# Optimization experiments

Hardware: AMD Instinct MI355X
Metric: run time of the kernel (lower is better)

## Reference

```python
import jax, jax.numpy as jnp
import numpy as np

D = 128            # actual_dim / embed_dim
DM = 2 * D         # d_model
HID = 2 * DM       # LSTMCell hidden size
NSYM = 200000
PAD = NSYM
B = 4096
S = 5
NB = 64
STEPS = 4
EPS = 1e-6


def setup_inputs() -> dict:
    key = jax.random.key(0)
    ks = jax.random.split(key, 24)
    def rn(k, sh, scale=0.02):
        return jax.random.normal(k, sh, dtype=jnp.float32) * scale
    emb = rn(ks[10], (NSYM + 1, D)).at[PAD].set(0.0)  # padding row zeroed
    inp = {
        'query': jax.random.randint(ks[0], (B, 2), 0, NSYM),
        'support': jax.random.randint(ks[1], (S, 2), 0, NSYM),
        'q_l_conn': jax.random.randint(ks[2], (B, NB, 2), 0, NSYM),
        'q_l_deg': jax.random.randint(ks[3], (B,), 0, NB),
        'q_r_conn': jax.random.randint(ks[4], (B, NB, 2), 0, NSYM),
        'q_r_deg': jax.random.randint(ks[5], (B,), 0, NB),
        's_l_conn': jax.random.randint(ks[6], (S, NB, 2), 0, NSYM),
        's_l_deg': jax.random.randint(ks[7], (S,), 0, NB),
        's_r_conn': jax.random.randint(ks[8], (S, NB, 2), 0, NSYM),
        's_r_deg': jax.random.randint(ks[9], (S,), 0, NB),
        'emb': emb,
        'gcn_w': rn(ks[11], (D, 2 * D)),
        'gcn_bias': jnp.zeros((D,), jnp.float32),
        'proj1_w': rn(ks[12], (2 * DM, DM)),
        'proj1_b': jnp.zeros((2 * DM,), jnp.float32),
        'proj2_w': rn(ks[13], (DM, 2 * DM)),
        'proj2_b': jnp.zeros((DM,), jnp.float32),
        'ln_g': jnp.ones((DM,), jnp.float32),
        'ln_b': jnp.zeros((DM,), jnp.float32),
        'w_ih': rn(ks[14], (4 * HID, DM)),
        'w_hh': rn(ks[15], (4 * HID, HID)),
        'b_ih': jnp.zeros((4 * HID,), jnp.float32),
        'b_hh': jnp.zeros((4 * HID,), jnp.float32),
    }
    return inp


def _neighbor_encoder(conn, deg, emb, gcn_w, gcn_bias):
    # conn: [N, NB, 2] ids (rel, ent); deg: [N]
    rel = emb[conn[:, :, 0]]                     # [N, NB, D] gather
    ent = emb[conn[:, :, 1]]                     # [N, NB, D] gather
    x = jnp.concatenate([rel, ent], axis=-1)     # [N, NB, 2D]
    out = jnp.einsum('bnd,kd->bnk', x, gcn_w) + gcn_bias  # [N, NB, D]
    denom = jnp.maximum(deg, 1).astype(out.dtype)[:, None]
    return jnp.tanh(out.sum(axis=1) / denom)     # [N, D]


def _support_encoder(x, proj1_w, proj1_b, proj2_w, proj2_b, ln_g, ln_b):
    residual = x
    h = jax.nn.relu(x @ proj1_w.T + proj1_b)
    h = h @ proj2_w.T + proj2_b
    z = h + residual
    mu = z.mean(axis=-1, keepdims=True)
    sigma = jnp.std(z, axis=-1, keepdims=True, ddof=1)
    return ln_g * (z - mu) / (sigma + EPS) + ln_b


def _query_encoder(support_vec, query, w_ih, w_hh, b_ih, b_hh):
    # support_vec: [DM] (single support prototype); query: [B, DM]
    bsz = query.shape[0]
    h_r = jnp.zeros((bsz, HID), query.dtype)
    c = jnp.zeros((bsz, HID), query.dtype)
    xW = query @ w_ih.T + b_ih  # invariant across steps
    h = query
    for _ in range(STEPS):
        gates = xW + h_r @ w_hh.T + b_hh
        i, f, g, o = jnp.split(gates, 4, axis=-1)
        c = jax.nn.sigmoid(f) * c + jax.nn.sigmoid(i) * jnp.tanh(g)
        h_cell = jax.nn.sigmoid(o) * jnp.tanh(c)
        h = query + h_cell[:, :DM]
        # attention over a single support row: softmax of one logit == 1
        r = jnp.broadcast_to(support_vec[None, :], h.shape)
        h_r = jnp.concatenate([h, r], axis=-1)
    return h


def reference(query, support, q_l_conn, q_l_deg, q_r_conn, q_r_deg,
              s_l_conn, s_l_deg, s_r_conn, s_r_deg,
              emb, gcn_w, gcn_bias, proj1_w, proj1_b, proj2_w, proj2_b,
              ln_g, ln_b, w_ih, w_hh, b_ih, b_hh):
    ql = _neighbor_encoder(q_l_conn, q_l_deg, emb, gcn_w, gcn_bias)
    qr = _neighbor_encoder(q_r_conn, q_r_deg, emb, gcn_w, gcn_bias)
    sl = _neighbor_encoder(s_l_conn, s_l_deg, emb, gcn_w, gcn_bias)
    sr = _neighbor_encoder(s_r_conn, s_r_deg, emb, gcn_w, gcn_bias)
    query_nb = jnp.concatenate([ql, qr], axis=-1)    # [B, DM]
    support_nb = jnp.concatenate([sl, sr], axis=-1)  # [S, DM]
    se = lambda x: _support_encoder(x, proj1_w, proj1_b, proj2_w, proj2_b, ln_g, ln_b)
    support_g = se(support_nb).mean(axis=0)          # [DM]
    query_g = se(query_nb)                            # [B, DM]
    query_f = _query_encoder(support_g, query_g, w_ih, w_hh, b_ih, b_hh)
    qn = query_f / jnp.maximum(jnp.linalg.norm(query_f, axis=-1, keepdims=True), 1e-12)
    sn = support_g / jnp.maximum(jnp.linalg.norm(support_g), 1e-12)
    return qn @ sn                                    # [B] matching scores
```

## Files before the change

kernel.cpp:

```cpp
#include <hip/hip_runtime.h>

#define BQ 4096
#define NS 5

typedef __attribute__((ext_vector_type(8))) short bf16x8;
typedef __attribute__((ext_vector_type(4))) float f32x4;
typedef unsigned short ushortT;

#define WS_QNB    0
#define WS_Z      1048576
#define WS_QG     2097152
#define WS_XW     3145728
#define WS_CBUF   5242880
#define WS_XS     6291456
#define WS_H1B    7348224
#define WS_ABF    7872512
#define WS_HB1    8134656
#define WS_P1B    8396800
#define WS_P2B    8462336
#define WS_WIHB   8527872
#define WS_WHHB   8658944
#define WS_GWB    8790016
#define WS_SNB    8806400
#define WS_H1G    8807680
#define WS_ZB     8810240
#define WS_SG     8811520
#define WS_SN     8811776
#define WS_SWL    8812032
#define WS_BL     8813056

__device__ __forceinline__ float wave_allreduce(float v) {
#pragma unroll
  for (int off = 32; off > 0; off >>= 1) v += __shfl_xor(v, off, 64);
  return v;
}
__device__ __forceinline__ float block_allreduce(float v, float* buf) {
  v = wave_allreduce(v);
  __syncthreads();
  if ((threadIdx.x & 63) == 0) buf[threadIdx.x >> 6] = v;
  __syncthreads();
  return buf[0] + buf[1] + buf[2] + buf[3];
}
__device__ __forceinline__ float sigm(float x) { return 1.0f / (1.0f + expf(-x)); }
__device__ __forceinline__ ushortT f2bf(float f) {
  unsigned int u = __float_as_uint(f);
  unsigned int r = (u + 0x7fffu + ((u >> 16) & 1u)) >> 16;
  return (ushortT)r;
}
__device__ __forceinline__ float bf2f(ushortT u) {
  return __uint_as_float(((unsigned int)u) << 16);
}
__device__ __forceinline__ float dot4(float4 a, float4 b) {
  return a.x * b.x + a.y * b.y + a.z * b.z + a.w * b.w;
}

__global__ void k_pack(const float* __restrict__ w_ih, const float* __restrict__ w_hh,
                       const float* __restrict__ p1w, const float* __restrict__ p2w,
                       const float* __restrict__ gcn_w,
                       const float* __restrict__ b_ih, const float* __restrict__ b_hh,
                       ushortT* __restrict__ p1b16, ushortT* __restrict__ p2b16,
                       ushortT* __restrict__ wihb, ushortT* __restrict__ whhb,
                       ushortT* __restrict__ gwb, float* __restrict__ bL) {
  const int stride = gridDim.x * blockDim.x;
  const int gid = blockIdx.x * blockDim.x + threadIdx.x;
  for (int i = gid; i < 131072; i += stride) p1b16[i] = f2bf(p1w[i]);
  for (int i = gid; i < 131072; i += stride) p2b16[i] = f2bf(p2w[i]);
  for (int i = gid; i < 262144; i += stride) {
    int n = i >> 8, k = i & 255;
    int j = (n >> 2) + 512 * (n & 3);
    wihb[i] = f2bf(w_ih[j * 256 + k]);
    whhb[i] = f2bf(w_hh[j * 512 + k]);
  }
  for (int i = gid; i < 32768; i += stride) gwb[i] = f2bf(gcn_w[i]);
  for (int i = gid; i < 1024; i += stride) {
    int j = (i >> 2) + 512 * (i & 3);
    bL[i] = b_ih[j] + b_hh[j];
  }
}

__global__ __launch_bounds__(256) void k_gather(
    const int* __restrict__ qlc, const int* __restrict__ qrc,
    const int* __restrict__ slc, const int* __restrict__ src_,
    const float* __restrict__ emb, ushortT* __restrict__ XS) {
  const int r = blockIdx.x;
  const int b = r >> 1, side = r & 1;
  const int t = threadIdx.x;
  const int* cg;
  if (b < BQ) cg = (side ? qrc : qlc) + (size_t)b * 128;
  else        cg = (side ? src_ : slc) + (size_t)(b - BQ) * 128;
  __shared__ int connS[128];
  __shared__ __align__(16) float part[8][132];
  if (t < 128) connS[t] = cg[t];
  __syncthreads();
  const int s = t >> 5, l = t & 31;
  const float4* emb4 = (const float4*)emb;
  float4 acc = make_float4(0.f, 0.f, 0.f, 0.f);
#pragma unroll
  for (int kb = 0; kb < 2; kb++) {
    int im[8];
#pragma unroll
    for (int k = 0; k < 8; k++) im[k] = connS[(kb * 8 + k) * 8 + s];
    float4 v[8];
#pragma unroll
    for (int k = 0; k < 8; k++) v[k] = emb4[(size_t)im[k] * 32 + l];
#pragma unroll
    for (int k = 0; k < 8; k++) {
      acc.x += v[k].x; acc.y += v[k].y; acc.z += v[k].z; acc.w += v[k].w;
    }
  }
  *(float4*)&part[s][l * 4] = acc;
  __syncthreads();
  const int hf = t >> 7, dd = t & 127;
  float sum = part[hf][dd] + part[2 + hf][dd] + part[4 + hf][dd] + part[6 + hf][dd];
  XS[(size_t)r * 256 + t] = f2bf(sum);
}

__global__ __launch_bounds__(256) void k_gcn(
    const ushortT* __restrict__ XS, const ushortT* __restrict__ gwb,
    const float* __restrict__ gcn_bias,
    const int* __restrict__ qld, const int* __restrict__ qrd,
    const int* __restrict__ sld, const int* __restrict__ srd,
    float* __restrict__ qnb, float* __restrict__ snb, ushortT* __restrict__ xq) {
  __shared__ short As[64 * 40];
  __shared__ short Bs[128 * 40];
  __shared__ int degl[32], degr[32];
  const int t = threadIdx.x;
  const int row0 = blockIdx.x * 64;
  if (t < 32) {
    int b = (row0 >> 1) + t;
    int dl = 1, dr = 1;
    if (b < BQ) { dl = qld[b]; dr = qrd[b]; }
    else if (b < BQ + NS) { dl = sld[b - BQ]; dr = srd[b - BQ]; }
    degl[t] = (dl > 0) ? dl : 1;
    degr[t] = (dr > 0) ? dr : 1;
  }
  const int wave = t >> 6, lane = t & 63;
  const int wm = wave >> 1, wn = wave & 1, quad = lane >> 4, mr = lane & 15;
  f32x4 acc[2][4];
#pragma unroll
  for (int mi = 0; mi < 2; mi++)
#pragma unroll
    for (int ni = 0; ni < 4; ni++) acc[mi][ni] = (f32x4){0.f, 0.f, 0.f, 0.f};
  const int arow = t >> 2, akc = t & 3;
  for (int k0 = 0; k0 < 256; k0 += 32) {
    float4 av = *(const float4*)(XS + (size_t)(row0 + arow) * 256 + k0 + akc * 8);
    float4 bv0 = *(const float4*)(gwb + (size_t)arow * 256 + k0 + akc * 8);
    float4 bv1 = *(const float4*)(gwb + (size_t)(64 + arow) * 256 + k0 + akc * 8);
    __syncthreads();
    *(float4*)&As[arow * 40 + akc * 8] = av;
    *(float4*)&Bs[arow * 40 + akc * 8] = bv0;
    *(float4*)&Bs[(64 + arow) * 40 + akc * 8] = bv1;
    __syncthreads();
    bf16x8 af[2], bfr[4];
#pragma unroll
    for (int mi = 0; mi < 2; mi++)
      af[mi] = *(const bf16x8*)&As[(wm * 32 + mi * 16 + mr) * 40 + quad * 8];
#pragma unroll
    for (int ni = 0; ni < 4; ni++)
      bfr[ni] = *(const bf16x8*)&Bs[(wn * 64 + ni * 16 + mr) * 40 + quad * 8];
#pragma unroll
    for (int mi = 0; mi < 2; mi++)
#pragma unroll
      for (int ni = 0; ni < 4; ni++)
        acc[mi][ni] = __builtin_amdgcn_mfma_f32_16x16x32_bf16(af[mi], bfr[ni], acc[mi][ni], 0, 0, 0);
  }
#pragma unroll
  for (int mi = 0; mi < 2; mi++) {
#pragma unroll
    for (int ni = 0; ni < 4; ni++) {
      const int col = wn * 64 + ni * 16 + mr;
      const int rb = row0 + wm * 32 + mi * 16 + quad * 4;
      const float bs = 64.0f * gcn_bias[col];
#pragma unroll
      for (int reg = 0; reg < 4; reg++) {
        const int row = rb + reg;
        const int b = row >> 1, side = row & 1;
        if (b >= BQ + NS) continue;
        const int li = (row >> 1) - (row0 >> 1);
        const int deg = side ? degr[li] : degl[li];
        float val = tanhf((acc[mi][ni][reg] + bs) / (float)deg);
        if (b < BQ) {
          const size_t o = (size_t)b * 256 + side * 128 + col;
          qnb[o] = val;
          xq[o] = f2bf(val);
        } else {
          snb[(size_t)(b - BQ) * 256 + side * 128 + col] = val;
        }
      }
    }
  }
}

__global__ __launch_bounds__(256) void k_sup1(
    const float* __restrict__ snb, const float* __restrict__ p1w,
    const float* __restrict__ p1b, float* __restrict__ h1g) {
  const int w = blockIdx.x * 4 + (threadIdx.x >> 6);
  const int lane = threadIdx.x & 63;
  const int r = w >> 9, j = w & 511;
  float4 x = *(const float4*)&snb[r * 256 + lane * 4];
  float4 wv = *(const float4*)&p1w[(size_t)j * 256 + lane * 4];
  float s = wave_allreduce(dot4(x, wv));
  if (lane == 0) h1g[r * 512 + j] = fmaxf(s + p1b[j], 0.f);
}

__global__ __launch_bounds__(256) void k_sup2(
    const float* __restrict__ snb, const float* __restrict__ h1g,
    const float* __restrict__ p2w, const float* __restrict__ p2b,
    float* __restrict__ zb) {
  const int w = blockIdx.x * 4 + (threadIdx.x >> 6);
  const int lane = threadIdx.x & 63;
  const int r = w >> 8, tt = w & 255;
  float4 h0 = *(const float4*)&h1g[r * 512 + lane * 4];
  float4 h1 = *(const float4*)&h1g[r * 512 + 256 + lane * 4];
  float4 w0 = *(const float4*)&p2w[(size_t)tt * 512 + lane * 4];
  float4 w1 = *(const float4*)&p2w[(size_t)tt * 512 + 256 + lane * 4];
  float s = wave_allreduce(dot4(h0, w0) + dot4(h1, w1));
  if (lane == 0) zb[r * 256 + tt] = s + p2b[tt] + snb[r * 256 + tt];
}

__global__ __launch_bounds__(256) void k_sup3(
    const float* __restrict__ zb, const float* __restrict__ ln_g,
    const float* __restrict__ ln_b, float* __restrict__ sg, float* __restrict__ sn) {
  const int t = threadIdx.x;
  __shared__ float rbuf[4];
  float acc = 0.f;
  for (int r = 0; r < NS; r++) {
    float z = zb[r * 256 + t];
    float s = block_allreduce(z, rbuf);
    float mu = s * (1.f / 256.f);
    float dz = z - mu;
    float s2 = block_allreduce(dz * dz, rbuf);
    float rstd = 1.f / (sqrtf(s2 * (1.f / 255.f)) + 1e-6f);
    acc += ln_g[t] * dz * rstd + ln_b[t];
    __syncthreads();
  }
  float g = acc * (1.f / (float)NS);
  sg[t] = g;
  float n2 = block_allreduce(g * g, rbuf);
  sn[t] = g / fmaxf(sqrtf(n2), 1e-12f);
}

__global__ __launch_bounds__(256) void k_sup4(
    const float* __restrict__ sg, const float* __restrict__ w_hh,
    float* __restrict__ sWl) {
  const int n = blockIdx.x * 4 + (threadIdx.x >> 6);
  const int lane = threadIdx.x & 63;
  const int j = (n >> 2) + 512 * (n & 3);
  float4 x = *(const float4*)&sg[lane * 4];
  float4 wv = *(const float4*)&w_hh[(size_t)j * 512 + 256 + lane * 4];
  float s = wave_allreduce(dot4(x, wv));
  if (lane == 0) sWl[n] = s;
}

__global__ __launch_bounds__(256) void k_gemm(
    const ushortT* __restrict__ A, const ushortT* __restrict__ B,
    const float* __restrict__ bias, const float* __restrict__ aux,
    float* __restrict__ outf, ushortT* __restrict__ outb,
    int K, int N, int nbn, int mode) {
  __shared__ short As[64 * 40];
  __shared__ short Bs[128 * 40];
  const int t = threadIdx.x;
  const int bn = blockIdx.x % nbn, bm = blockIdx.x / nbn;
  const int row0 = bm * 64, col0 = bn * 128;
  const int wave = t >> 6, lane = t & 63;
  const int wm = wave >> 1, wn = wave & 1, quad = lane >> 4, mr = lane & 15;
  f32x4 acc[2][4];
#pragma unroll
  for (int mi = 0; mi < 2; mi++)
#pragma unroll
    for (int ni = 0; ni < 4; ni++) acc[mi][ni] = (f32x4){0.f, 0.f, 0.f, 0.f};
  const int arow = t >> 2, akc = t & 3;
  for (int k0 = 0; k0 < K; k0 += 32) {
    float4 av = *(const float4*)(A + (size_t)(row0 + arow) * K + k0 + akc * 8);
    float4 bv0 = *(const float4*)(B + (size_t)(col0 + arow) * K + k0 + akc * 8);
    float4 bv1 = *(const float4*)(B + (size_t)(col0 + 64 + arow) * K + k0 + akc * 8);
    __syncthreads();
    *(float4*)&As[arow * 40 + akc * 8] = av;
    *(float4*)&Bs[arow * 40 + akc * 8] = bv0;
    *(float4*)&Bs[(64 + arow) * 40 + akc * 8] = bv1;
    __syncthreads();
    bf16x8 af[2], bfr[4];
#pragma unroll
    for (int mi = 0; mi < 2; mi++)
      af[mi] = *(const bf16x8*)&As[(wm * 32 + mi * 16 + mr) * 40 + quad * 8];
#pragma unroll
    for (int ni = 0; ni < 4; ni++)
      bfr[ni] = *(const bf16x8*)&Bs[(wn * 64 + ni * 16 + mr) * 40 + quad * 8];
#pragma unroll
    for (int mi = 0; mi < 2; mi++)
#pragma unroll
      for (int ni = 0; ni < 4; ni++)
        acc[mi][ni] = __builtin_amdgcn_mfma_f32_16x16x32_bf16(af[mi], bfr[ni], acc[mi][ni], 0, 0, 0);
  }
#pragma unroll
  for (int mi = 0; mi < 2; mi++) {
#pragma unroll
    for (int ni = 0; ni < 4; ni++) {
      const int col = col0 + wn * 64 + ni * 16 + mr;
      const int rb = row0 + wm * 32 + mi * 16 + quad * 4;
      const float bs = bias[col];
#pragma unroll
      for (int reg = 0; reg < 4; reg++) {
        const int row = rb + reg;
        const size_t off = (size_t)row * N + col;
        float v = acc[mi][ni][reg];
        if (mode == 0) outb[off] = f2bf(fmaxf(v + bs, 0.f));
        else outf[off] = v + bs + aux[off];
      }
    }
  }
}

__global__ __launch_bounds__(256) void k_gemm_lstm(
    const ushortT* __restrict__ A, const ushortT* __restrict__ B,
    const float* __restrict__ bL, const float* __restrict__ sWl,
    const float* __restrict__ qg, ushortT* __restrict__ xwb,
    float* __restrict__ cbuf, ushortT* __restrict__ hb_out, int phase) {
  __shared__ short As[64 * 40];
  __shared__ short Bs[128 * 40];
  __shared__ __align__(16) float Cs[64 * 132];
  const int t = threadIdx.x;
  const int bn = blockIdx.x & 7, bm = blockIdx.x >> 3;
  const int row0 = bm * 64, col0 = bn * 128;
  const int wave = t >> 6, lane = t & 63;
  const int wm = wave >> 1, wn = wave & 1, quad = lane >> 4, mr = lane & 15;
  f32x4 acc[2][4];
#pragma unroll
  for (int mi = 0; mi < 2; mi++)
#pragma unroll
    for (int ni = 0; ni < 4; ni++) acc[mi][ni] = (f32x4){0.f, 0.f, 0.f, 0.f};
  const int arow = t >> 2, akc = t & 3;
  for (int k0 = 0; k0 < 256; k0 += 32) {
    float4 av = *(const float4*)(A + (size_t)(row0 + arow) * 256 + k0 + akc * 8);
    float4 bv0 = *(const float4*)(B + (size_t)(col0 + arow) * 256 + k0 + akc * 8);
    float4 bv1 = *(const float4*)(B + (size_t)(col0 + 64 + arow) * 256 + k0 + akc * 8);
    __syncthreads();
    *(float4*)&As[arow * 40 + akc * 8] = av;
    *(float4*)&Bs[arow * 40 + akc * 8] = bv0;
    *(float4*)&Bs[(64 + arow) * 40 + akc * 8] = bv1;
    __syncthreads();
    bf16x8 af[2], bfr[4];
#pragma unroll
    for (int mi = 0; mi < 2; mi++)
      af[mi] = *(const bf16x8*)&As[(wm * 32 + mi * 16 + mr) * 40 + quad * 8];
#pragma unroll
    for (int ni = 0; ni < 4; ni++)
      bfr[ni] = *(const bf16x8*)&Bs[(wn * 64 + ni * 16 + mr) * 40 + quad * 8];
#pragma unroll
    for (int mi = 0; mi < 2; mi++)
#pragma unroll
      for (int ni = 0; ni < 4; ni++)
        acc[mi][ni] = __builtin_amdgcn_mfma_f32_16x16x32_bf16(af[mi], bfr[ni], acc[mi][ni], 0, 0, 0);
  }
#pragma unroll
  for (int mi = 0; mi < 2; mi++)
#pragma unroll
    for (int ni = 0; ni < 4; ni++)
#pragma unroll
      for (int reg = 0; reg < 4; reg++)
        Cs[(wm * 32 + mi * 16 + quad * 4 + reg) * 132 + wn * 64 + ni * 16 + mr] =
            acc[mi][ni][reg];
  __syncthreads();
  const int u = t & 31, grp = t >> 5;
  const int ugl = bn * 32 + u;
#pragma unroll
  for (int i = 0; i < 8; i++) {
    const int rl = grp * 8 + i;
    const int row = row0 + rl;
    const size_t o = (size_t)row * 256 + ugl;
    float4 gv = *(const float4*)&Cs[rl * 132 + u * 4];
    if (phase == 0) {
      float4 bb = *(const float4*)&bL[col0 + u * 4];
      gv.x += bb.x; gv.y += bb.y; gv.z += bb.z; gv.w += bb.w;
      float c0 = sigm(gv.x) * tanhf(gv.z);
      float h = qg[o] + sigm(gv.w) * tanhf(c0);
      cbuf[o] = c0;
      hb_out[o] = f2bf(h);
      float4 sv = *(const float4*)&sWl[col0 + u * 4];
      ushort4 xo;
      xo.x = f2bf(gv.x + sv.x); xo.y = f2bf(gv.y + sv.y);
      xo.z = f2bf(gv.z + sv.z); xo.w = f2bf(gv.w + sv.w);
      *(ushort4*)&xwb[(size_t)row * 1024 + col0 + u * 4] = xo;
    } else {
      ushort4 xv = *(const ushort4*)&xwb[(size_t)row * 1024 + col0 + u * 4];
      gv.x += bf2f(xv.x); gv.y += bf2f(xv.y);
      gv.z += bf2f(xv.z); gv.w += bf2f(xv.w);
      float c = sigm(gv.y) * cbuf[o] + sigm(gv.x) * tanhf(gv.z);
      float h = qg[o] + sigm(gv.w) * tanhf(c);
      if (phase == 2) {
        cbuf[o] = h;
      } else {
        cbuf[o] = c;
        hb_out[o] = f2bf(h);
      }
    }
  }
}

__global__ __launch_bounds__(256) void k_ln(
    const float* __restrict__ Z, const float* __restrict__ ln_g,
    const float* __restrict__ ln_b, float* __restrict__ qg, ushortT* __restrict__ qgb) {
  const int t = threadIdx.x;
  const int row = blockIdx.x * 4 + (t >> 6);
  const int lane = t & 63;
  float4 z = *(const float4*)&Z[(size_t)row * 256 + lane * 4];
  float s = wave_allreduce(z.x + z.y + z.z + z.w);
  float mu = s * (1.f / 256.f);
  float dx = z.x - mu, dy = z.y - mu, dz = z.z - mu, dw = z.w - mu;
  float s2 = wave_allreduce(dx * dx + dy * dy + dz * dz + dw * dw);
  float rstd = 1.f / (sqrtf(s2 * (1.f / 255.f)) + 1e-6f);
  float4 g = *(const float4*)&ln_g[lane * 4];
  float4 bb = *(const float4*)&ln_b[lane * 4];
  float4 o;
  o.x = g.x * dx * rstd + bb.x;
  o.y = g.y * dy * rstd + bb.y;
  o.z = g.z * dz * rstd + bb.z;
  o.w = g.w * dw * rstd + bb.w;
  *(float4*)&qg[(size_t)row * 256 + lane * 4] = o;
  ushort4 u;
  u.x = f2bf(o.x); u.y = f2bf(o.y); u.z = f2bf(o.z); u.w = f2bf(o.w);
  *(ushort4*)&qgb[(size_t)row * 256 + lane * 4] = u;
}

__global__ __launch_bounds__(256) void k_out(
    const float* __restrict__ hf, const float* __restrict__ sn, float* __restrict__ out) {
  const int t = threadIdx.x;
  const int row = blockIdx.x * 4 + (t >> 6);
  const int lane = t & 63;
  float4 h = *(const float4*)&hf[(size_t)row * 256 + lane * 4];
  float4 s = *(const float4*)&sn[lane * 4];
  float dt = wave_allreduce(dot4(h, s));
  float nr = wave_allreduce(dot4(h, h));
  if (lane == 0) out[row] = dt / fmaxf(sqrtf(nr), 1e-12f);
}

extern "C" void kernel_launch(void* const* d_in, const int* in_sizes, int n_in,
                              void* d_out, int out_size, void* d_ws, size_t ws_size,
                              hipStream_t stream) {
  const int* q_l_conn = (const int*)d_in[2];
  const int* q_l_deg  = (const int*)d_in[3];
  const int* q_r_conn = (const int*)d_in[4];
  const int* q_r_deg  = (const int*)d_in[5];
  const int* s_l_conn = (const int*)d_in[6];
  const int* s_l_deg  = (const int*)d_in[7];
  const int* s_r_conn = (const int*)d_in[8];
  const int* s_r_deg  = (const int*)d_in[9];
  const float* emb      = (const float*)d_in[10];
  const float* gcn_w    = (const float*)d_in[11];
  const float* gcn_bias = (const float*)d_in[12];
  const float* proj1_w  = (const float*)d_in[13];
  const float* proj1_b  = (const float*)d_in[14];
  const float* proj2_w  = (const float*)d_in[15];
  const float* proj2_b  = (const float*)d_in[16];
  const float* ln_g     = (const float*)d_in[17];
  const float* ln_b     = (const float*)d_in[18];
  const float* w_ih     = (const float*)d_in[19];
  const float* w_hh     = (const float*)d_in[20];
  const float* b_ih     = (const float*)d_in[21];
  const float* b_hh     = (const float*)d_in[22];

  float* ws = (float*)d_ws;
  float* qnb   = ws + WS_QNB;
  float* Z     = ws + WS_Z;
  float* qg    = ws + WS_QG;
  ushortT* xwb = (ushortT*)(ws + WS_XW);
  float* cbuf  = ws + WS_CBUF;
  ushortT* XS    = (ushortT*)(ws + WS_XS);
  ushortT* h1b   = (ushortT*)(ws + WS_H1B);
  ushortT* abf   = (ushortT*)(ws + WS_ABF);
  ushortT* hb1   = (ushortT*)(ws + WS_HB1);
  ushortT* p1b16 = (ushortT*)(ws + WS_P1B);
  ushortT* p2b16 = (ushortT*)(ws + WS_P2B);
  ushortT* wihb  = (ushortT*)(ws + WS_WIHB);
  ushortT* whhb  = (ushortT*)(ws + WS_WHHB);
  ushortT* gwb   = (ushortT*)(ws + WS_GWB);
  float* snb   = ws + WS_SNB;
  float* h1g   = ws + WS_H1G;
  float* zb    = ws + WS_ZB;
  float* sg    = ws + WS_SG;
  float* sn    = ws + WS_SN;
  float* sWl   = ws + WS_SWL;
  float* bL    = ws + WS_BL;
  float* out   = (float*)d_out;

  hipLaunchKernelGGL(k_pack, dim3(512), dim3(256), 0, stream,
                     w_ih, w_hh, proj1_w, proj2_w, gcn_w, b_ih, b_hh,
                     p1b16, p2b16, wihb, whhb, gwb, bL);
  hipLaunchKernelGGL(k_gather, dim3(2 * (BQ + NS)), dim3(256), 0, stream,
                     q_l_conn, q_r_conn, s_l_conn, s_r_conn, emb, XS);
  hipLaunchKernelGGL(k_gcn, dim3(129), dim3(256), 0, stream,
                     XS, gwb, gcn_bias, q_l_deg, q_r_deg, s_l_deg, s_r_deg,
                     qnb, snb, abf);
  hipLaunchKernelGGL(k_sup1, dim3(640), dim3(256), 0, stream, snb, proj1_w, proj1_b, h1g);
  hipLaunchKernelGGL(k_sup2, dim3(320), dim3(256), 0, stream, snb, h1g, proj2_w, proj2_b, zb);
  hipLaunchKernelGGL(k_sup3, dim3(1), dim3(256), 0, stream, zb, ln_g, ln_b, sg, sn);
  hipLaunchKernelGGL(k_sup4, dim3(256), dim3(256), 0, stream, sg, w_hh, sWl);
  hipLaunchKernelGGL(k_gemm, dim3(64 * 4), dim3(256), 0, stream,
                     abf, p1b16, proj1_b, (const float*)nullptr, (float*)nullptr, h1b,
                     256, 512, 4, 0);
  hipLaunchKernelGGL(k_gemm, dim3(64 * 2), dim3(256), 0, stream,
                     h1b, p2b16, proj2_b, qnb, Z, (ushortT*)nullptr,
                     512, 256, 2, 1);
  hipLaunchKernelGGL(k_ln, dim3(BQ / 4), dim3(256), 0, stream, Z, ln_g, ln_b, qg, abf);
  hipLaunchKernelGGL(k_gemm_lstm, dim3(512), dim3(256), 0, stream,
                     abf, wihb, bL, sWl, qg, xwb, cbuf, hb1, 0);
  hipLaunchKernelGGL(k_gemm_lstm, dim3(512), dim3(256), 0, stream,
                     hb1, whhb, bL, sWl, qg, xwb, cbuf, abf, 1);
  hipLaunchKernelGGL(k_gemm_lstm, dim3(512), dim3(256), 0, stream,
                     abf, whhb, bL, sWl, qg, xwb, cbuf, hb1, 1);
  hipLaunchKernelGGL(k_gemm_lstm, dim3(512), dim3(256), 0, stream,
                     hb1, whhb, bL, sWl, qg, xwb, cbuf, (ushortT*)nullptr, 2);
  hipLaunchKernelGGL(k_out, dim3(BQ / 4), dim3(256), 0, stream, cbuf, sn, out);
}
```

Baseline: 364.0 us.

## Fuse weight packing into gather and support-encoder chain into GCN tail block

The weight-packing kernel is folded into the gather kernel as 512 extra blocks. The four support-side kernels (two projections, LayerNorm with mean, and the w_hh projection) are merged into the final block of the GCN kernel, which keeps the support rows in shared memory. The goal is to remove five kernel launches and the global round-trips of the small intermediates. The cost is that one workgroup now does roughly 2 MB of weight reads and all the support arithmetic serially, using per-thread row-strided loads. That adds a long tail to the GCN kernel that every later kernel waits on.

```diff
diff --git a/kernel.cpp b/kernel.cpp
--- a/kernel.cpp
+++ b/kernel.cpp
@@ -54,37 +54,38 @@
   return a.x * b.x + a.y * b.y + a.z * b.z + a.w * b.w;
 }
 
-__global__ void k_pack(const float* __restrict__ w_ih, const float* __restrict__ w_hh,
-                       const float* __restrict__ p1w, const float* __restrict__ p2w,
-                       const float* __restrict__ gcn_w,
-                       const float* __restrict__ b_ih, const float* __restrict__ b_hh,
-                       ushortT* __restrict__ p1b16, ushortT* __restrict__ p2b16,
-                       ushortT* __restrict__ wihb, ushortT* __restrict__ whhb,
-                       ushortT* __restrict__ gwb, float* __restrict__ bL) {
-  const int stride = gridDim.x * blockDim.x;
-  const int gid = blockIdx.x * blockDim.x + threadIdx.x;
-  for (int i = gid; i < 131072; i += stride) p1b16[i] = f2bf(p1w[i]);
-  for (int i = gid; i < 131072; i += stride) p2b16[i] = f2bf(p2w[i]);
-  for (int i = gid; i < 262144; i += stride) {
-    int n = i >> 8, k = i & 255;
-    int j = (n >> 2) + 512 * (n & 3);
-    wihb[i] = f2bf(w_ih[j * 256 + k]);
-    whhb[i] = f2bf(w_hh[j * 512 + k]);
-  }
-  for (int i = gid; i < 32768; i += stride) gwb[i] = f2bf(gcn_w[i]);
-  for (int i = gid; i < 1024; i += stride) {
-    int j = (i >> 2) + 512 * (i & 3);
-    bL[i] = b_ih[j] + b_hh[j];
-  }
-}
-
 __global__ __launch_bounds__(256) void k_gather(
     const int* __restrict__ qlc, const int* __restrict__ qrc,
     const int* __restrict__ slc, const int* __restrict__ src_,
-    const float* __restrict__ emb, ushortT* __restrict__ XS) {
+    const float* __restrict__ emb, ushortT* __restrict__ XS,
+    const float* __restrict__ w_ih, const float* __restrict__ w_hh,
+    const float* __restrict__ p1w, const float* __restrict__ p2w,
+    const float* __restrict__ gcn_w,
+    const float* __restrict__ b_ih, const float* __restrict__ b_hh,
+    ushortT* __restrict__ p1b16, ushortT* __restrict__ p2b16,
+    ushortT* __restrict__ wihb, ushortT* __restrict__ whhb,
+    ushortT* __restrict__ gwb, float* __restrict__ bL) {
   const int r = blockIdx.x;
+  const int t = threadIdx.x;
+  if (r >= 2 * (BQ + NS)) {
+    const int gid = (r - 2 * (BQ + NS)) * 256 + t;
+    const int stride = 512 * 256;
+    for (int i = gid; i < 131072; i += stride) p1b16[i] = f2bf(p1w[i]);
+    for (int i = gid; i < 131072; i += stride) p2b16[i] = f2bf(p2w[i]);
+    for (int i = gid; i < 262144; i += stride) {
+      int n = i >> 8, k = i & 255;
+      int j = (n >> 2) + 512 * (n & 3);
+      wihb[i] = f2bf(w_ih[j * 256 + k]);
+      whhb[i] = f2bf(w_hh[j * 512 + k]);
+    }
+    for (int i = gid; i < 32768; i += stride) gwb[i] = f2bf(gcn_w[i]);
+    for (int i = gid; i < 1024; i += stride) {
+      int j = (i >> 2) + 512 * (i & 3);
+      bL[i] = b_ih[j] + b_hh[j];
+    }
+    return;
+  }
   const int b = r >> 1, side = r & 1;
-  const int t = threadIdx.x;
   const int* cg;
   if (b < BQ) cg = (side ? qrc : qlc) + (size_t)b * 128;
   else        cg = (side ? src_ : slc) + (size_t)(b - BQ) * 128;
@@ -120,10 +121,19 @@
     const float* __restrict__ gcn_bias,
     const int* __restrict__ qld, const int* __restrict__ qrd,
     const int* __restrict__ sld, const int* __restrict__ srd,
-    float* __restrict__ qnb, float* __restrict__ snb, ushortT* __restrict__ xq) {
+    float* __restrict__ qnb, ushortT* __restrict__ xq,
+    const float* __restrict__ p1w, const float* __restrict__ p1b,
+    const float* __restrict__ p2w, const float* __restrict__ p2b,
+    const float* __restrict__ ln_g, const float* __restrict__ ln_b,
+    const float* __restrict__ w_hh,
+    float* __restrict__ sn_out, float* __restrict__ sWl) {
   __shared__ short As[64 * 40];
   __shared__ short Bs[128 * 40];
   __shared__ int degl[32], degr[32];
+  __shared__ __align__(16) float snbS[5][256];
+  __shared__ __align__(16) float h1S[5][512];
+  __shared__ __align__(16) float sgS[256];
+  __shared__ float rbuf[4];
   const int t = threadIdx.x;
   const int row0 = blockIdx.x * 64;
   if (t < 32) {
@@ -184,72 +194,70 @@
           qnb[o] = val;
           xq[o] = f2bf(val);
         } else {
-          snb[(size_t)(b - BQ) * 256 + side * 128 + col] = val;
+          snbS[b - BQ][side * 128 + col] = val;
         }
       }
     }
   }
-}
-
-__global__ __launch_bounds__(256) void k_sup1(
-    const float* __restrict__ snb, const float* __restrict__ p1w,
-    const float* __restrict__ p1b, float* __restrict__ h1g) {
-  const int w = blockIdx.x * 4 + (threadIdx.x >> 6);
-  const int lane = threadIdx.x & 63;
-  const int r = w >> 9, j = w & 511;
-  float4 x = *(const float4*)&snb[r * 256 + lane * 4];
-  float4 wv = *(const float4*)&p1w[(size_t)j * 256 + lane * 4];
-  float s = wave_allreduce(dot4(x, wv));
-  if (lane == 0) h1g[r * 512 + j] = fmaxf(s + p1b[j], 0.f);
-}
-
-__global__ __launch_bounds__(256) void k_sup2(
-    const float* __restrict__ snb, const float* __restrict__ h1g,
-    const float* __restrict__ p2w, const float* __restrict__ p2b,
-    float* __restrict__ zb) {
-  const int w = blockIdx.x * 4 + (threadIdx.x >> 6);
-  const int lane = threadIdx.x & 63;
-  const int r = w >> 8, tt = w & 255;
-  float4 h0 = *(const float4*)&h1g[r * 512 + lane * 4];
-  float4 h1 = *(const float4*)&h1g[r * 512 + 256 + lane * 4];
-  float4 w0 = *(const float4*)&p2w[(size_t)tt * 512 + lane * 4];
-  float4 w1 = *(const float4*)&p2w[(size_t)tt * 512 + 256 + lane * 4];
-  float s = wave_allreduce(dot4(h0, w0) + dot4(h1, w1));
-  if (lane == 0) zb[r * 256 + tt] = s + p2b[tt] + snb[r * 256 + tt];
-}
-
-__global__ __launch_bounds__(256) void k_sup3(
-    const float* __restrict__ zb, const float* __restrict__ ln_g,
-    const float* __restrict__ ln_b, float* __restrict__ sg, float* __restrict__ sn) {
-  const int t = threadIdx.x;
-  __shared__ float rbuf[4];
-  float acc = 0.f;
-  for (int r = 0; r < NS; r++) {
-    float z = zb[r * 256 + t];
-    float s = block_allreduce(z, rbuf);
-    float mu = s * (1.f / 256.f);
-    float dz = z - mu;
-    float s2 = block_allreduce(dz * dz, rbuf);
-    float rstd = 1.f / (sqrtf(s2 * (1.f / 255.f)) + 1e-6f);
-    acc += ln_g[t] * dz * rstd + ln_b[t];
-    __syncthreads();
-  }
-  float g = acc * (1.f / (float)NS);
-  sg[t] = g;
-  float n2 = block_allreduce(g * g, rbuf);
-  sn[t] = g / fmaxf(sqrtf(n2), 1e-12f);
-}
-
-__global__ __launch_bounds__(256) void k_sup4(
-    const float* __restrict__ sg, const float* __restrict__ w_hh,
-    float* __restrict__ sWl) {
-  const int n = blockIdx.x * 4 + (threadIdx.x >> 6);
-  const int lane = threadIdx.x & 63;
-  const int j = (n >> 2) + 512 * (n & 3);
-  float4 x = *(const float4*)&sg[lane * 4];
-  float4 wv = *(const float4*)&w_hh[(size_t)j * 512 + 256 + lane * 4];
-  float s = wave_allreduce(dot4(x, wv));
-  if (lane == 0) sWl[n] = s;
+  if (row0 == 2 * BQ) {
+    __syncthreads();
+#pragma unroll
+    for (int jj = 0; jj < 2; jj++) {
+      const int j = jj * 256 + t;
+      float a5[5] = {0.f, 0.f, 0.f, 0.f, 0.f};
+      for (int kk = 0; kk < 64; kk++) {
+        float4 wv = *(const float4*)&p1w[(size_t)j * 256 + kk * 4];
+#pragma unroll
+        for (int rr = 0; rr < 5; rr++) {
+          float4 xv = *(const float4*)&snbS[rr][kk * 4];
+          a5[rr] += dot4(xv, wv);
+        }
+      }
+      const float bj = p1b[j];
+#pragma unroll
+      for (int rr = 0; rr < 5; rr++) h1S[rr][j] = fmaxf(a5[rr] + bj, 0.f);
+    }
+    __syncthreads();
+    float zr[5] = {0.f, 0.f, 0.f, 0.f, 0.f};
+    for (int kk = 0; kk < 128; kk++) {
+      float4 wv = *(const float4*)&p2w[(size_t)t * 512 + kk * 4];
+#pragma unroll
+      for (int rr = 0; rr < 5; rr++) {
+        float4 hv = *(const float4*)&h1S[rr][kk * 4];
+        zr[rr] += dot4(hv, wv);
+      }
+    }
+    const float bt = p2b[t];
+#pragma unroll
+    for (int rr = 0; rr < 5; rr++) zr[rr] += bt + snbS[rr][t];
+    float accg = 0.f;
+#pragma unroll
+    for (int rr = 0; rr < 5; rr++) {
+      float s = block_allreduce(zr[rr], rbuf);
+      float mu = s * (1.f / 256.f);
+      float dz = zr[rr] - mu;
+      float s2 = block_allreduce(dz * dz, rbuf);
+      float rstd = 1.f / (sqrtf(s2 * (1.f / 255.f)) + 1e-6f);
+      accg += ln_g[t] * dz * rstd + ln_b[t];
+      __syncthreads();
+    }
+    float g = accg * (1.f / (float)NS);
+    sgS[t] = g;
+    float n2 = block_allreduce(g * g, rbuf);
+    sn_out[t] = g / fmaxf(sqrtf(n2), 1e-12f);
+    __syncthreads();
+    float a4[4] = {0.f, 0.f, 0.f, 0.f};
+    for (int kk = 0; kk < 64; kk++) {
+      float4 sv = *(const float4*)&sgS[kk * 4];
+#pragma unroll
+      for (int c = 0; c < 4; c++) {
+        float4 wv = *(const float4*)&w_hh[(size_t)(t + 512 * c) * 512 + 256 + kk * 4];
+        a4[c] += dot4(sv, wv);
+      }
+    }
+#pragma unroll
+    for (int c = 0; c < 4; c++) sWl[4 * t + c] = a4[c];
+  }
 }
 
 __global__ __launch_bounds__(256) void k_gemm(
@@ -407,8 +415,11 @@
   float s = wave_allreduce(z.x + z.y + z.z + z.w);
   float mu = s * (1.f / 256.f);
   float dx = z.x - mu, dy = z.y - mu, dz = z.z - mu, dw = z.w - mu;
-  float s2 = wave_allreduce(dx * dx + dy * dy + dz * dz + dw * dw);
-  float rstd = 1.f / (sqrtf(s2 * (1.f / 255.f)) + 1e-6f);
+  float rstd;
+  {
+    float s2 = wave_allreduce(dx * dx + dy * dy + dz * dz + dw * dw);
+    rstd = 1.f / (sqrtf(s2 * (1.f / 255.f)) + 1e-6f);
+  }
   float4 g = *(const float4*)&ln_g[lane * 4];
   float4 bb = *(const float4*)&ln_b[lane * 4];
   float4 o;
@@ -474,27 +485,20 @@
   ushortT* wihb  = (ushortT*)(ws + WS_WIHB);
   ushortT* whhb  = (ushortT*)(ws + WS_WHHB);
   ushortT* gwb   = (ushortT*)(ws + WS_GWB);
-  float* snb   = ws + WS_SNB;
-  float* h1g   = ws + WS_H1G;
-  float* zb    = ws + WS_ZB;
-  float* sg    = ws + WS_SG;
   float* sn    = ws + WS_SN;
   float* sWl   = ws + WS_SWL;
   float* bL    = ws + WS_BL;
   float* out   = (float*)d_out;
 
-  hipLaunchKernelGGL(k_pack, dim3(512), dim3(256), 0, stream,
+  hipLaunchKernelGGL(k_gather, dim3(2 * (BQ + NS) + 512), dim3(256), 0, stream,
+                     q_l_conn, q_r_conn, s_l_conn, s_r_conn, emb, XS,
                      w_ih, w_hh, proj1_w, proj2_w, gcn_w, b_ih, b_hh,
                      p1b16, p2b16, wihb, whhb, gwb, bL);
-  hipLaunchKernelGGL(k_gather, dim3(2 * (BQ + NS)), dim3(256), 0, stream,
-                     q_l_conn, q_r_conn, s_l_conn, s_r_conn, emb, XS);
   hipLaunchKernelGGL(k_gcn, dim3(129), dim3(256), 0, stream,
                      XS, gwb, gcn_bias, q_l_deg, q_r_deg, s_l_deg, s_r_deg,
-                     qnb, snb, abf);
-  hipLaunchKernelGGL(k_sup1, dim3(640), dim3(256), 0, stream, snb, proj1_w, proj1_b, h1g);
-  hipLaunchKernelGGL(k_sup2, dim3(320), dim3(256), 0, stream, snb, h1g, proj2_w, proj2_b, zb);
-  hipLaunchKernelGGL(k_sup3, dim3(1), dim3(256), 0, stream, zb, ln_g, ln_b, sg, sn);
-  hipLaunchKernelGGL(k_sup4, dim3(256), dim3(256), 0, stream, sg, w_hh, sWl);
+                     qnb, abf,
+                     proj1_w, proj1_b, proj2_w, proj2_b, ln_g, ln_b, w_hh,
+                     sn, sWl);
   hipLaunchKernelGGL(k_gemm, dim3(64 * 4), dim3(256), 0, stream,
                      abf, p1b16, proj1_b, (const float*)nullptr, (float*)nullptr, h1b,
                      256, 512, 4, 0);
```

New measurement: 432.9 us. 19.0% more time.
